# Kernel tuning notes

Hardware: AMD Instinct MI355X
Metric: run time of the kernel (lower is better)

## Reference

```python
import jax, jax.numpy as jnp
import numpy as np

NB = 4
QN = -(2 ** (NB - 1))   # -8
QP = 2 ** (NB - 1) - 1  # 7
EPS = 1e-5


def _grad_scale(x, g):
    # forward: x, backward: grad * g (LSQ gradient scaling)
    return x * g + jax.lax.stop_gradient(x - x * g)


def _round_pass(x):
    # round with straight-through estimator
    return x + jax.lax.stop_gradient(jnp.round(x) - x)


def _lsq(v, alpha, qn, qp):
    # LSQ fake quantize-dequantize with learnable step size alpha
    g = 1.0 / np.sqrt(v.size * qp)
    a = _grad_scale(alpha, g)
    return _round_pass(jnp.clip(v / a, qn, qp)) * a


def _bn(x, g, b, m, v):
    # eval-mode BatchNorm2d over channel dim of NCHW
    s = (g * jax.lax.rsqrt(v + EPS))[None, :, None, None]
    return (x - m[None, :, None, None]) * s + b[None, :, None, None]


def _conv(x, w, stride, pad, groups):
    return jax.lax.conv_general_dilated(
        x, w, (stride, stride), pad,
        dimension_numbers=('NCHW', 'OIHW', 'NCHW'),
        feature_group_count=groups)


def setup_inputs() -> dict:
    key = jax.random.key(0)
    ks = jax.random.split(key, 4)
    inp, oup, hid = 96, 96, 576
    B, H, W = 32, 28, 28
    d = {}
    d['x'] = jax.random.normal(ks[0], (B, inp, H, W), jnp.float32)
    d['w1'] = jax.random.normal(ks[1], (hid, inp, 1, 1), jnp.float32) * 0.1
    d['w2'] = jax.random.normal(ks[2], (hid, 1, 3, 3), jnp.float32) * 0.1
    d['w3'] = jax.random.normal(ks[3], (oup, hid, 1, 1), jnp.float32) * 0.1
    for i, c in zip((1, 2, 3), (hid, hid, oup)):
        d[f'aw{i}'] = jnp.full((1,), 0.05, jnp.float32)  # weight step size
        d[f'ax{i}'] = jnp.full((1,), 0.5, jnp.float32)   # activation step size
        d[f'g{i}'] = jnp.ones((c,), jnp.float32)
        d[f'b{i}'] = jnp.zeros((c,), jnp.float32)
        d[f'm{i}'] = jnp.zeros((c,), jnp.float32)
        d[f'v{i}'] = jnp.ones((c,), jnp.float32)
    return d


def reference(x, w1, w2, w3, aw1, ax1, g1, b1, m1, v1,
              aw2, ax2, g2, b2, m2, v2, aw3, ax3, g3, b3, m3, v3):
    hid = w1.shape[0]
    # 1x1 expand conv (LSQ on activation and weight)
    h = _conv(_lsq(x, ax1, QN, QP), _lsq(w1, aw1, QN, QP), 1, [(0, 0), (0, 0)], 1)
    h = jnp.clip(_bn(h, g1, b1, m1, v1), 0.0, 6.0)
    # 3x3 depthwise conv, stride 1
    h = _conv(_lsq(h, ax2, QN, QP), _lsq(w2, aw2, QN, QP), 1, [(1, 1), (1, 1)], hid)
    h = jnp.clip(_bn(h, g2, b2, m2, v2), 0.0, 6.0)
    # 1x1 project conv
    h = _conv(_lsq(h, ax3, QN, QP), _lsq(w3, aw3, QN, QP), 1, [(0, 0), (0, 0)], 1)
    h = _bn(h, g3, b3, m3, v3)
    # identity residual (stride==1 and inp==oup)
    return x + h
```

## Files before the change

### kernel.cpp

```cpp
#include <hip/hip_runtime.h>

#define EPSF 1e-5f

typedef int    int4v   __attribute__((ext_vector_type(4)));
typedef float  float4v __attribute__((ext_vector_type(4)));

#define W1P_OFF  0
#define W3P_OFF  55296
#define W2D_OFF  110592
#define S1B1_OFF 202752
#define S2B2_OFF 207360
#define S3B3_OFF 211968

#define H1S 296
#define H2S 600

__device__ __forceinline__ float lsq_q(float v, float a) {
    float t = v / a;
    t = fminf(fmaxf(t, -8.0f), 7.0f);
    return rintf(t);
}

__device__ __forceinline__ long q8pack_w(const float* w, int base, const int* idx, float a) {
    unsigned long long v = 0;
    #pragma unroll
    for (int j = 0; j < 8; ++j) {
        int q = (int)lsq_q(w[base + idx[j]], a);
        v |= (unsigned long long)(q & 255) << (8 * j);
    }
    return (long)v;
}

__global__ __launch_bounds__(256)
void prep_w(const float* __restrict__ w1, const float* __restrict__ w2,
            const float* __restrict__ w3,
            const float* aw1, const float* ax1, const float* ax2,
            const float* aw2, const float* ax3, const float* aw3,
            const float* __restrict__ g1, const float* __restrict__ b1,
            const float* __restrict__ m1, const float* __restrict__ v1,
            const float* __restrict__ g2, const float* __restrict__ b2,
            const float* __restrict__ m2, const float* __restrict__ v2,
            const float* __restrict__ g3, const float* __restrict__ b3,
            const float* __restrict__ m3, const float* __restrict__ v3,
            long* __restrict__ w1p, long* __restrict__ w3p,
            long* __restrict__ w2d,
            float* __restrict__ s1b1, float* __restrict__ s2b2,
            float* __restrict__ s3b3) {
    int id = blockIdx.x * 256 + threadIdx.x;
    const int lin[8] = {0, 1, 2, 3, 4, 5, 6, 7};
    if (id < 6912) {
        int l = id & 63, t = id >> 6;
        int kc = t % 3, ct = t / 3;
        int co = ct * 16 + (l & 15);
        int ci0 = kc * 32 + (l >> 4) * 8;
        w1p[id] = q8pack_w(w1, co * 96 + ci0, lin, aw1[0]);
    } else if (id < 13824) {
        int i = id - 6912;
        int l = i & 63, t = i >> 6;
        int kc = t % 18, ct = t / 18;
        int co = ct * 16 + (l & 15);
        int ci0 = kc * 32 + (l >> 4) * 8;
        w3p[i] = q8pack_w(w3, co * 576 + ci0, lin, aw3[0]);
    } else if (id < 25344) {
        int i = id - 13824;
        int l = i & 63, t = i >> 6;
        int kc = t % 5, ct = t / 5;
        int quad = l >> 4, m = l & 15;
        int tap = kc * 2 + (quad >> 1);
        unsigned long long v = 0;
        if (tap <= 8) {
            int mh = m - (quad & 1) * 8;
            if (mh >= 0 && mh < 8) {
                int j = (mh >> 1) | ((mh & 1) << 2);
                int q = (int)lsq_q(w2[(ct * 16 + m) * 9 + tap], aw2[0]);
                v = (unsigned long long)(unsigned)(q & 255) << (8 * j);
            }
        }
        w2d[i] = (long)v;
    } else if (id < 25920) {
        int c = id - 25344;
        float s = g1[c] / sqrtf(v1[c] + EPSF);
        float A = aw1[0] * ax1[0];
        float inv = 1.0f / ax2[0];
        s1b1[c] = A * s * inv;
        s1b1[576 + c] = (b1[c] - m1[c] * s) * inv;
    } else if (id < 26496) {
        int c = id - 25920;
        float s = g2[c] / sqrtf(v2[c] + EPSF);
        float A = ax2[0] * aw2[0];
        float inv = 1.0f / ax3[0];
        s2b2[c] = A * s * inv;
        s2b2[576 + c] = (b2[c] - m2[c] * s) * inv;
    } else if (id < 26592) {
        int c = id - 26496;
        float s = g3[c] / sqrtf(v3[c] + EPSF);
        float A = ax3[0] * aw3[0];
        s3b3[c] = A * s;
        s3b3[96 + c] = b3[c] - m3[c] * s;
    }
}

__global__ __launch_bounds__(448, 4)
void fused_k(const float* __restrict__ x, const long* __restrict__ w1p,
             const long* __restrict__ w2d, const long* __restrict__ w3p,
             const float* __restrict__ ax1,
             const float* __restrict__ s1b1, const float* __restrict__ s2b2,
             const float* __restrict__ s3b3, float* __restrict__ out) {
    __shared__ __align__(16) signed char h1[120 * H1S];
    __shared__ __align__(16) signed char h2[64 * H2S];
    const int tid = threadIdx.x;
    const int w = tid >> 6, l = tid & 63;
    const int quad = l >> 4, c16 = l & 15;
    const int qh = quad >> 1, ql = quad & 1;
    const int b = blockIdx.x;
    const int r0 = blockIdx.y * 2;

    for (int i = tid; i < 120 * H1S / 16; i += 448)
        ((int4v*)h1)[i] = (int4v){0, 0, 0, 0};
    __syncthreads();

    {
        const int lp = w * 16 + c16;
        const int row = lp / 28, col = lp - (lp / 28) * 28;
        const int img_row = r0 - 1 + row;
        const bool valid = (unsigned)img_row < 28u;
        const int p = min(max(img_row, 0), 27) * 28 + col;
        const float inv1 = 1.0f / ax1[0];

        long bfr[3];
        #pragma unroll
        for (int kc = 0; kc < 3; ++kc) {
            const float* xs = x + (b * 96 + kc * 32 + quad * 8) * 784 + p;
            unsigned long long v = 0;
            #pragma unroll
            for (int j = 0; j < 8; ++j) {
                float t = xs[j * 784] * inv1;
                t = fminf(fmaxf(t, -8.0f), 7.0f);
                int q = (int)rintf(t);
                v |= (unsigned long long)(q & 255) << (8 * j);
            }
            bfr[kc] = (long)v;
        }
        const int pos_h = row * 30 + col + 1;
        #pragma unroll 4
        for (int ct = 0; ct < 36; ++ct) {
            int4v acc; acc[0] = 0; acc[1] = 0; acc[2] = 0; acc[3] = 0;
            #pragma unroll
            for (int kc = 0; kc < 3; ++kc)
                acc = __builtin_amdgcn_mfma_i32_16x16x32_i8(
                    w1p[(ct * 3 + kc) * 64 + l], bfr[kc], acc, 0, 0, 0);
            const int co0 = ct * 16 + quad * 4;
            float4v S = *(const float4v*)(s1b1 + co0);
            float4v B = *(const float4v*)(s1b1 + 576 + co0);
            int pk = 0;
            #pragma unroll
            for (int r = 0; r < 4; ++r) {
                float t = fmaf((float)acc[r], S[r], B[r]);
                t = fminf(fmaxf(t, 0.0f), 7.0f);
                pk |= ((int)rintf(t)) << (4 * r);
            }
            if (valid)
                *(unsigned short*)(h1 + pos_h * H1S + (co0 >> 1)) = (unsigned short)pk;
        }
    }
    __syncthreads();

    for (int t = w; t < 144; t += 7) {
        const int pt = t / 36, ct = t - (t / 36) * 36;
        const int pos = pt * 16 + c16;
        const int posc = min(pos, 55);
        const int row_in = posc / 28, col = posc - (posc / 28) * 28;
        const int choff = ct * 8 + ql * 4;
        int4v acc; acc[0] = 0; acc[1] = 0; acc[2] = 0; acc[3] = 0;
        #pragma unroll
        for (int kc = 0; kc < 5; ++kc) {
            int tap = kc * 2 + qh;
            tap = min(tap, 8);
            const int dh = tap / 3 - 1, dc = tap - (tap / 3) * 3 - 1;
            const int pos_h = (row_in + 1 + dh) * 30 + (col + 1 + dc);
            const unsigned v = *(const unsigned*)(h1 + pos_h * H1S + choff);
            const unsigned lo = v & 0x0F0F0F0Fu;
            const unsigned hi = (v >> 4) & 0x0F0F0F0Fu;
            const long bf = (long)(((unsigned long long)hi << 32) | lo);
            acc = __builtin_amdgcn_mfma_i32_16x16x32_i8(
                w2d[(ct * 5 + kc) * 64 + l], bf, acc, 0, 0, 0);
        }
        if (pos < 56) {
            const int c0 = ct * 16 + quad * 4;
            float4v S = *(const float4v*)(s2b2 + c0);
            float4v B = *(const float4v*)(s2b2 + 576 + c0);
            int pk = 0;
            #pragma unroll
            for (int r = 0; r < 4; ++r) {
                float tt = fmaf((float)acc[r], S[r], B[r]);
                tt = fminf(fmaxf(tt, 0.0f), 7.0f);
                pk |= ((int)rintf(tt)) << (8 * r);
            }
            *(int*)(h2 + pos * H2S + c0) = pk;
        }
    }
    __syncthreads();

    for (int t = w; t < 24; t += 7) {
        const int nt = t / 6, ct = t - (t / 6) * 6;
        int4v acc; acc[0] = 0; acc[1] = 0; acc[2] = 0; acc[3] = 0;
        const signed char* arow = h2 + (nt * 16 + c16) * H2S + quad * 8;
        #pragma unroll 6
        for (int kc = 0; kc < 18; ++kc)
            acc = __builtin_amdgcn_mfma_i32_16x16x32_i8(
                *(const long*)(arow + kc * 32),
                w3p[(ct * 18 + kc) * 64 + l], acc, 0, 0, 0);
        const int nloc = nt * 16 + quad * 4;
        if (nloc < 56) {
            const int co = ct * 16 + c16;
            const float S = s3b3[co], Bv = s3b3[96 + co];
            const int off = (b * 96 + co) * 784 + r0 * 28 + nloc;
            const float4v xr = *(const float4v*)(x + off);
            float4v o;
            #pragma unroll
            for (int r = 0; r < 4; ++r)
                o[r] = fmaf((float)acc[r], S, Bv) + xr[r];
            *(float4v*)(out + off) = o;
        }
    }
}

extern "C" void kernel_launch(void* const* d_in, const int* in_sizes, int n_in,
                              void* d_out, int out_size, void* d_ws, size_t ws_size,
                              hipStream_t stream) {
    const float* x   = (const float*)d_in[0];
    const float* w1  = (const float*)d_in[1];
    const float* w2  = (const float*)d_in[2];
    const float* w3  = (const float*)d_in[3];
    const float* aw1 = (const float*)d_in[4];
    const float* ax1 = (const float*)d_in[5];
    const float* g1  = (const float*)d_in[6];
    const float* b1  = (const float*)d_in[7];
    const float* m1  = (const float*)d_in[8];
    const float* v1  = (const float*)d_in[9];
    const float* aw2 = (const float*)d_in[10];
    const float* ax2 = (const float*)d_in[11];
    const float* g2  = (const float*)d_in[12];
    const float* b2  = (const float*)d_in[13];
    const float* m2  = (const float*)d_in[14];
    const float* v2  = (const float*)d_in[15];
    const float* aw3 = (const float*)d_in[16];
    const float* ax3 = (const float*)d_in[17];
    const float* g3  = (const float*)d_in[18];
    const float* b3  = (const float*)d_in[19];
    const float* m3  = (const float*)d_in[20];
    const float* v3  = (const float*)d_in[21];

    char* ws = (char*)d_ws;
    long* w1p = (long*)(ws + W1P_OFF);
    long* w3p = (long*)(ws + W3P_OFF);
    long* w2d = (long*)(ws + W2D_OFF);
    float* s1b1 = (float*)(ws + S1B1_OFF);
    float* s2b2 = (float*)(ws + S2B2_OFF);
    float* s3b3 = (float*)(ws + S3B3_OFF);

    float* out = (float*)d_out;

    prep_w<<<104, 256, 0, stream>>>(w1, w2, w3, aw1, ax1, ax2, aw2, ax3, aw3,
                                    g1, b1, m1, v1, g2, b2, m2, v2, g3, b3, m3, v3,
                                    w1p, w3p, w2d, s1b1, s2b2, s3b3);
    dim3 grid(32, 14);
    fused_k<<<grid, 448, 0, stream>>>(x, w1p, w2d, w3p, ax1, s1b1, s2b2, s3b3, out);
}
```

Baseline: 147.5 us.

## Overlap input loads with LDS zeroing, use magic-number rounding, hoist residual loads

Input activations are now loaded into registers before the shared-memory zeroing and barrier, so global load latency overlaps the clearing. Quantization switches from divide, clamp and rint to an fma plus magic-constant integer clamp, and to fmed3 plus magic-add rounding for the BN outputs. Residual x and the BN3 scale and bias are loaded before the projection MFMA loop so their latency hides behind it. The prep kernel launch is also reshaped to 128-thread blocks. The changes cost more live registers, and the magic-number rounding relies on round-to-nearest-even behaviour matching rintf.

Measured after the change: 149.1 us. Within noise of the previous version (+1.1%).

```diff
diff --git a/kernel.cpp b/kernel.cpp
--- a/kernel.cpp
+++ b/kernel.cpp
@@ -1,6 +1,9 @@
 #include <hip/hip_runtime.h>
 
 #define EPSF 1e-5f
+#define MAGICF 12582912.0f
+#define MLO 0x4B3FFFF8
+#define MHI 0x4B400007
 
 typedef int    int4v   __attribute__((ext_vector_type(4)));
 typedef float  float4v __attribute__((ext_vector_type(4)));
@@ -31,7 +34,7 @@
     return (long)v;
 }
 
-__global__ __launch_bounds__(256)
+__global__ __launch_bounds__(128)
 void prep_w(const float* __restrict__ w1, const float* __restrict__ w2,
             const float* __restrict__ w3,
             const float* aw1, const float* ax1, const float* ax2,
@@ -46,7 +49,7 @@
             long* __restrict__ w2d,
             float* __restrict__ s1b1, float* __restrict__ s2b2,
             float* __restrict__ s3b3) {
-    int id = blockIdx.x * 256 + threadIdx.x;
+    int id = blockIdx.x * 128 + threadIdx.x;
     const int lin[8] = {0, 1, 2, 3, 4, 5, 6, 7};
     if (id < 6912) {
         int l = id & 63, t = id >> 6;
@@ -115,10 +118,6 @@
     const int b = blockIdx.x;
     const int r0 = blockIdx.y * 2;
 
-    for (int i = tid; i < 120 * H1S / 16; i += 448)
-        ((int4v*)h1)[i] = (int4v){0, 0, 0, 0};
-    __syncthreads();
-
     {
         const int lp = w * 16 + c16;
         const int row = lp / 28, col = lp - (lp / 28) * 28;
@@ -127,17 +126,27 @@
         const int p = min(max(img_row, 0), 27) * 28 + col;
         const float inv1 = 1.0f / ax1[0];
 
+        float xv[3][8];
+        #pragma unroll
+        for (int kc = 0; kc < 3; ++kc) {
+            const float* xs = x + (b * 96 + kc * 32 + quad * 8) * 784 + p;
+            #pragma unroll
+            for (int j = 0; j < 8; ++j) xv[kc][j] = xs[j * 784];
+        }
+
+        for (int i = tid; i < 120 * H1S / 16; i += 448)
+            ((int4v*)h1)[i] = (int4v){0, 0, 0, 0};
+        __syncthreads();
+
         long bfr[3];
         #pragma unroll
         for (int kc = 0; kc < 3; ++kc) {
-            const float* xs = x + (b * 96 + kc * 32 + quad * 8) * 784 + p;
             unsigned long long v = 0;
             #pragma unroll
             for (int j = 0; j < 8; ++j) {
-                float t = xs[j * 784] * inv1;
-                t = fminf(fmaxf(t, -8.0f), 7.0f);
-                int q = (int)rintf(t);
-                v |= (unsigned long long)(q & 255) << (8 * j);
+                int qi = __float_as_int(fmaf(xv[kc][j], inv1, MAGICF));
+                qi = min(max(qi, MLO), MHI);
+                v |= (unsigned long long)(qi & 255) << (8 * j);
             }
             bfr[kc] = (long)v;
         }
@@ -154,10 +163,10 @@
             float4v B = *(const float4v*)(s1b1 + 576 + co0);
             int pk = 0;
             #pragma unroll
-            for (int r = 0; r < 4; ++r) {
-                float t = fmaf((float)acc[r], S[r], B[r]);
-                t = fminf(fmaxf(t, 0.0f), 7.0f);
-                pk |= ((int)rintf(t)) << (4 * r);
+            for (int r2 = 0; r2 < 4; ++r2) {
+                float t = fmaf((float)acc[r2], S[r2], B[r2]);
+                t = __builtin_amdgcn_fmed3f(t, 0.0f, 7.0f);
+                pk |= (__float_as_int(t + MAGICF) & 15) << (4 * r2);
             }
             if (valid)
                 *(unsigned short*)(h1 + pos_h * H1S + (co0 >> 1)) = (unsigned short)pk;
@@ -191,10 +200,10 @@
             float4v B = *(const float4v*)(s2b2 + 576 + c0);
             int pk = 0;
             #pragma unroll
-            for (int r = 0; r < 4; ++r) {
-                float tt = fmaf((float)acc[r], S[r], B[r]);
-                tt = fminf(fmaxf(tt, 0.0f), 7.0f);
-                pk |= ((int)rintf(tt)) << (8 * r);
+            for (int r2 = 0; r2 < 4; ++r2) {
+                float tt = fmaf((float)acc[r2], S[r2], B[r2]);
+                tt = __builtin_amdgcn_fmed3f(tt, 0.0f, 7.0f);
+                pk |= (__float_as_int(tt + MAGICF) & 255) << (8 * r2);
             }
             *(int*)(h2 + pos * H2S + c0) = pk;
         }
@@ -203,6 +212,11 @@
 
     for (int t = w; t < 24; t += 7) {
         const int nt = t / 6, ct = t - (t / 6) * 6;
+        const int nloc = nt * 16 + quad * 4;
+        const int co = ct * 16 + c16;
+        const int off = (b * 96 + co) * 784 + r0 * 28 + min(nloc, 52);
+        const float4v xr = *(const float4v*)(x + off);
+        const float S = s3b3[co], Bv = s3b3[96 + co];
         int4v acc; acc[0] = 0; acc[1] = 0; acc[2] = 0; acc[3] = 0;
         const signed char* arow = h2 + (nt * 16 + c16) * H2S + quad * 8;
         #pragma unroll 6
@@ -210,16 +224,11 @@
             acc = __builtin_amdgcn_mfma_i32_16x16x32_i8(
                 *(const long*)(arow + kc * 32),
                 w3p[(ct * 18 + kc) * 64 + l], acc, 0, 0, 0);
-        const int nloc = nt * 16 + quad * 4;
         if (nloc < 56) {
-            const int co = ct * 16 + c16;
-            const float S = s3b3[co], Bv = s3b3[96 + co];
-            const int off = (b * 96 + co) * 784 + r0 * 28 + nloc;
-            const float4v xr = *(const float4v*)(x + off);
             float4v o;
             #pragma unroll
-            for (int r = 0; r < 4; ++r)
-                o[r] = fmaf((float)acc[r], S, Bv) + xr[r];
+            for (int r2 = 0; r2 < 4; ++r2)
+                o[r2] = fmaf((float)acc[r2], S, Bv) + xr[r2];
             *(float4v*)(out + off) = o;
         }
     }
@@ -261,7 +270,7 @@
 
     float* out = (float*)d_out;
 
-    prep_w<<<104, 256, 0, stream>>>(w1, w2, w3, aw1, ax1, ax2, aw2, ax3, aw3,
+    prep_w<<<208, 128, 0, stream>>>(w1, w2, w3, aw1, ax1, ax2, aw2, ax3, aw3,
                                     g1, b1, m1, v1, g2, b2, m2, v2, g3, b3, m3, v3,
                                     w1p, w3p, w2d, s1b1, s2b2, s3b3);
     dim3 grid(32, 14);
```
